# Optimization experiments

Hardware: AMD Instinct MI355X
Metric: run time of the kernel (lower is better)

## Reference

```python
import jax, jax.numpy as jnp
import numpy as np

N_NODES = 100000
N_EDGES = 1600000
IN_FEATS, N_HIDDEN, N_CLASSES = 128, 128, 32


def setup_inputs() -> dict:
    key = jax.random.key(0)
    ks = jax.random.split(key, 9)
    x = jax.random.normal(ks[0], (N_NODES, IN_FEATS), dtype=jnp.float32)
    src = jax.random.randint(ks[1], (N_EDGES,), 0, N_NODES, dtype=jnp.int64)
    dst = jax.random.randint(ks[2], (N_EDGES,), 0, N_NODES, dtype=jnp.int64)
    s1 = 1.0 / np.sqrt(IN_FEATS)
    s2 = 1.0 / np.sqrt(N_HIDDEN)
    W1 = jax.random.uniform(ks[3], (IN_FEATS, N_HIDDEN), jnp.float32, -s1, s1)
    b1 = jnp.zeros((N_HIDDEN,), jnp.float32)
    W2 = jax.random.uniform(ks[4], (N_HIDDEN, N_HIDDEN), jnp.float32, -s2, s2)
    b2 = jnp.zeros((N_HIDDEN,), jnp.float32)
    W3 = jax.random.uniform(ks[5], (N_HIDDEN, N_CLASSES), jnp.float32, -s2, s2)
    b3 = jnp.zeros((N_CLASSES,), jnp.float32)
    return {"x": x, "W1": W1, "b1": b1, "W2": W2, "b2": b2, "W3": W3, "b3": b3,
            "src": src, "dst": dst}


def _norms(src, dst):
    ones = jnp.ones((src.shape[0],), jnp.float32)
    deg_out = jax.ops.segment_sum(ones, src, num_segments=N_NODES)
    deg_in = jax.ops.segment_sum(ones, dst, num_segments=N_NODES)
    inv_sqrt = lambda d: jnp.where(d > 0, jax.lax.rsqrt(jnp.maximum(d, 1.0)), 0.0)
    return inv_sqrt(deg_out), inv_sqrt(deg_in)


def _sgconv(h, W, b, src, dst, norm_src, norm_dst):
    # D^-1/2 A D^-1/2 h, then linear
    m = h * norm_src[:, None]          # scale by source (out-degree) norm
    msg = m[src]                        # [E, F] gather
    agg = jax.ops.segment_sum(msg, dst, num_segments=N_NODES)  # scatter-add
    agg = agg * norm_dst[:, None]
    return agg @ W + b


def reference(x, W1, b1, W2, b2, W3, b3, src, dst):
    norm_src, norm_dst = _norms(src, dst)
    h = _sgconv(x, W1, b1, src, dst, norm_src, norm_dst)
    h = jax.nn.relu(h)
    h = _sgconv(h, W2, b2, src, dst, norm_src, norm_dst)
    h = jax.nn.relu(h)
    h = _sgconv(h, W3, b3, src, dst, norm_src, norm_dst)
    return h
```

## Files before the change

kernel.cpp:

```cpp
#include <hip/hip_runtime.h>


constexpr int FEAT   = 128;
constexpr int STRIDE = 48;

typedef float f32x4 __attribute__((ext_vector_type(4)));
typedef short bf16x8 __attribute__((ext_vector_type(8)));

__device__ __forceinline__ unsigned short f2bf(float f) {
    unsigned int u = __builtin_bit_cast(unsigned int, f);
    unsigned int r = (u + 0x7FFFu + ((u >> 16) & 1u)) >> 16;
    return (unsigned short)r;
}
__device__ __forceinline__ float bflo(unsigned int u) {
    return __builtin_bit_cast(float, u << 16);
}
__device__ __forceinline__ float bfhi(unsigned int u) {
    return __builtin_bit_cast(float, u & 0xffff0000u);
}
__device__ __forceinline__ unsigned int pack2(float a, float b) {
    return (unsigned int)f2bf(a) | ((unsigned int)f2bf(b) << 16);
}

__global__ __launch_bounds__(256) void w1frag_kernel(const float* __restrict__ W1,
                                                     unsigned short* __restrict__ frag)
{
    constexpr int NC = 128;
    int idx = blockIdx.x * 256 + threadIdx.x;
    if (idx >= 8 * 4 * 64) return;
    int l  = idx & 63;
    int k0 = (idx >> 6) & 3;
    int n0 = idx >> 8;
    int kb = k0 * 32 + (l >> 4) * 8;
    int n  = n0 * 16 + (l & 15);
    const float* wp = W1 + (size_t)kb * NC + n;
    uint4 v;
    v.x = pack2(wp[0],      wp[NC]);
    v.y = pack2(wp[2 * NC], wp[3 * NC]);
    v.z = pack2(wp[4 * NC], wp[5 * NC]);
    v.w = pack2(wp[6 * NC], wp[7 * NC]);
    *reinterpret_cast<uint4*>(&frag[idx * 8]) = v;
}

__global__ __launch_bounds__(256) void degree_fill_xw1_kernel(
    const int* __restrict__ src, const int* __restrict__ dst,
    const float* __restrict__ x, const unsigned short* __restrict__ w1frag,
    int* __restrict__ deg_out, int* __restrict__ deg_in,
    int* __restrict__ csr_pad, unsigned short* __restrict__ xw1,
    int N, int E)
{
    const int tid = threadIdx.x;
    const int g = (int)blockIdx.x / 5;
    const int m = (int)blockIdx.x % 5;

    if (m != 4) {
        int e = (g * 4 + m) * 256 + tid;
        if (e < E) {
            int s = src[e];
            int d = dst[e];
            atomicAdd(&deg_out[s], 1);
            int pos = atomicAdd(&deg_in[d], 1);
            if (pos < STRIDE)
                csr_pad[(size_t)d * STRIDE + pos] = s;
        }
        return;
    }

    const int wave = tid >> 6, lane = tid & 63;
    const int rowbase = g * 64 + wave * 16;
    const int arow = min(rowbase + (lane & 15), N - 1);
    const int koff = (lane >> 4) * 8;

    bf16x8 a[4];
    #pragma unroll
    for (int k0 = 0; k0 < 4; ++k0) {
        const float* xp = x + (size_t)arow * 128 + k0 * 32 + koff;
        float4 f0 = *reinterpret_cast<const float4*>(xp);
        float4 f1 = *reinterpret_cast<const float4*>(xp + 4);
        union { unsigned int u[4]; bf16x8 v; } r;
        r.u[0] = pack2(f0.x, f0.y); r.u[1] = pack2(f0.z, f0.w);
        r.u[2] = pack2(f1.x, f1.y); r.u[3] = pack2(f1.z, f1.w);
        a[k0] = r.v;
    }

    f32x4 acc[8];
    #pragma unroll
    for (int n0 = 0; n0 < 8; ++n0) acc[n0] = (f32x4)0.f;
    #pragma unroll
    for (int k0 = 0; k0 < 4; ++k0) {
        #pragma unroll
        for (int n0 = 0; n0 < 8; ++n0) {
            bf16x8 b = *reinterpret_cast<const bf16x8*>(&w1frag[((n0 * 4 + k0) * 64 + lane) * 8]);
            acc[n0] = __builtin_amdgcn_mfma_f32_16x16x32_bf16(a[k0], b, acc[n0], 0, 0, 0);
        }
    }

    const int colbase = lane & 15;
    const int rowoff = (lane >> 4) * 4;
    #pragma unroll
    for (int r = 0; r < 4; ++r) {
        const int grow = rowbase + rowoff + r;
        if (grow < N) {
            unsigned short* op = xw1 + (size_t)grow * 128 + colbase;
            #pragma unroll
            for (int n0 = 0; n0 < 8; ++n0)
                op[n0 * 16] = f2bf(acc[n0][r]);
        }
    }
}

__global__ __launch_bounds__(256) void norm_kernel(const int* __restrict__ dout,
                                                   const int* __restrict__ din,
                                                   float* __restrict__ nsrc,
                                                   float* __restrict__ ndst, int N)
{
    int i = blockIdx.x * 256 + threadIdx.x;
    if (i < N) {
        int a = dout[i], b = din[i];
        nsrc[i] = (a > 0) ? rsqrtf((float)a) : 0.f;
        ndst[i] = (b > 0) ? rsqrtf((float)b) : 0.f;
    }
}

__global__ __launch_bounds__(256) void gather1_kernel(const unsigned short* __restrict__ xw1,
                                                      const float* __restrict__ nsrc,
                                                      const float* __restrict__ ndst,
                                                      const int* __restrict__ deg_in,
                                                      const int* __restrict__ csr_pad,
                                                      const float* __restrict__ b1,
                                                      unsigned short* __restrict__ hb1,
                                                      int N)
{
    const int node = blockIdx.x * 16 + (threadIdx.x >> 4);
    const int c = (threadIdx.x & 15) * 8;
    if (node >= N) return;
    const int* idx = csr_pad + (size_t)node * STRIDE;
    const int deg = min(deg_in[node], STRIDE);
    float4 a0 = make_float4(0.f, 0.f, 0.f, 0.f);
    float4 a1 = make_float4(0.f, 0.f, 0.f, 0.f);
    int j = 0;
    for (; j + 8 <= deg; j += 8) {
        int s[8];
        float ns[8];
        #pragma unroll
        for (int u = 0; u < 8; ++u) s[u] = idx[j + u];
        #pragma unroll
        for (int u = 0; u < 8; ++u) ns[u] = nsrc[s[u]];
        #pragma unroll
        for (int u = 0; u < 8; ++u) {
            uint4 v = *reinterpret_cast<const uint4*>(xw1 + (size_t)s[u] * 128 + c);
            a0.x = fmaf(bflo(v.x), ns[u], a0.x);
            a0.y = fmaf(bfhi(v.x), ns[u], a0.y);
            a0.z = fmaf(bflo(v.y), ns[u], a0.z);
            a0.w = fmaf(bfhi(v.y), ns[u], a0.w);
            a1.x = fmaf(bflo(v.z), ns[u], a1.x);
            a1.y = fmaf(bfhi(v.z), ns[u], a1.y);
            a1.z = fmaf(bflo(v.w), ns[u], a1.z);
            a1.w = fmaf(bfhi(v.w), ns[u], a1.w);
        }
    }
    for (; j < deg; ++j) {
        int s0 = idx[j];
        float n0 = nsrc[s0];
        uint4 v = *reinterpret_cast<const uint4*>(xw1 + (size_t)s0 * 128 + c);
        a0.x = fmaf(bflo(v.x), n0, a0.x);
        a0.y = fmaf(bfhi(v.x), n0, a0.y);
        a0.z = fmaf(bflo(v.y), n0, a0.z);
        a0.w = fmaf(bfhi(v.y), n0, a0.w);
        a1.x = fmaf(bflo(v.z), n0, a1.x);
        a1.y = fmaf(bfhi(v.z), n0, a1.y);
        a1.z = fmaf(bflo(v.w), n0, a1.z);
        a1.w = fmaf(bfhi(v.w), n0, a1.w);
    }
    const float nd = ndst[node];
    const float nsn = nsrc[node];
    const float* bp = b1 + c;
    float v0 = fmaxf(a0.x * nd + bp[0], 0.f) * nsn;
    float v1 = fmaxf(a0.y * nd + bp[1], 0.f) * nsn;
    float v2 = fmaxf(a0.z * nd + bp[2], 0.f) * nsn;
    float v3 = fmaxf(a0.w * nd + bp[3], 0.f) * nsn;
    float v4 = fmaxf(a1.x * nd + bp[4], 0.f) * nsn;
    float v5 = fmaxf(a1.y * nd + bp[5], 0.f) * nsn;
    float v6 = fmaxf(a1.z * nd + bp[6], 0.f) * nsn;
    float v7 = fmaxf(a1.w * nd + bp[7], 0.f) * nsn;
    uint4 o;
    o.x = pack2(v0, v1); o.y = pack2(v2, v3);
    o.z = pack2(v4, v5); o.w = pack2(v6, v7);
    *reinterpret_cast<uint4*>(hb1 + (size_t)node * 128 + c) = o;
}

__global__ __launch_bounds__(256) void gather128_kernel(const unsigned short* __restrict__ hb,
                                                        const float* __restrict__ ndst,
                                                        const int* __restrict__ deg_in,
                                                        const int* __restrict__ csr_pad,
                                                        unsigned short* __restrict__ aggb,
                                                        int N)
{
    const int node = blockIdx.x * 16 + (threadIdx.x >> 4);
    const int c = (threadIdx.x & 15) * 8;
    if (node >= N) return;
    const int* idx = csr_pad + (size_t)node * STRIDE;
    const int deg = min(deg_in[node], STRIDE);
    float4 a0 = make_float4(0.f, 0.f, 0.f, 0.f);
    float4 a1 = make_float4(0.f, 0.f, 0.f, 0.f);
    int j = 0;
    for (; j + 8 <= deg; j += 8) {
        int s[8];
        #pragma unroll
        for (int u = 0; u < 8; ++u) s[u] = idx[j + u];
        #pragma unroll
        for (int u = 0; u < 8; ++u) {
            uint4 v = *reinterpret_cast<const uint4*>(hb + (size_t)s[u] * 128 + c);
            a0.x += bflo(v.x); a0.y += bfhi(v.x);
            a0.z += bflo(v.y); a0.w += bfhi(v.y);
            a1.x += bflo(v.z); a1.y += bfhi(v.z);
            a1.z += bflo(v.w); a1.w += bfhi(v.w);
        }
    }
    for (; j < deg; ++j) {
        uint4 v = *reinterpret_cast<const uint4*>(hb + (size_t)idx[j] * 128 + c);
        a0.x += bflo(v.x); a0.y += bfhi(v.x);
        a0.z += bflo(v.y); a0.w += bfhi(v.y);
        a1.x += bflo(v.z); a1.y += bfhi(v.z);
        a1.z += bflo(v.w); a1.w += bfhi(v.w);
    }
    const float nd = ndst[node];
    uint4 o;
    o.x = pack2(a0.x * nd, a0.y * nd);
    o.y = pack2(a0.z * nd, a0.w * nd);
    o.z = pack2(a1.x * nd, a1.y * nd);
    o.w = pack2(a1.z * nd, a1.w * nd);
    *reinterpret_cast<uint4*>(aggb + (size_t)node * 128 + c) = o;
}

template<int NT, bool RELU, bool BIAS, bool SCALE>
__global__ __launch_bounds__(256) void mfma_gemm_kernel(
    const unsigned short* __restrict__ Ab,
    const float* __restrict__ W,
    const float* __restrict__ bias,
    const float* __restrict__ nsrc,
    unsigned short* __restrict__ Cb,
    int N)
{
    constexpr int NC = NT * 16;
    constexpr int SLD = (NC == 128) ? 136 : 32;
    __shared__ alignas(16) unsigned short Wl[NT * 4 * 64 * 8];
    __shared__ alignas(16) unsigned short Sc[4][16 * SLD];
    const int tid = threadIdx.x;

    for (int idx = tid; idx < NT * 4 * 64; idx += 256) {
        int l  = idx & 63;
        int k0 = (idx >> 6) & 3;
        int n0 = idx >> 8;
        int kb = k0 * 32 + (l >> 4) * 8;
        int n  = n0 * 16 + (l & 15);
        const float* wp = W + (size_t)kb * NC + n;
        uint4 v;
        v.x = pack2(wp[0],      wp[NC]);
        v.y = pack2(wp[2 * NC], wp[3 * NC]);
        v.z = pack2(wp[4 * NC], wp[5 * NC]);
        v.w = pack2(wp[6 * NC], wp[7 * NC]);
        *reinterpret_cast<uint4*>(&Wl[idx * 8]) = v;
    }
    __syncthreads();

    const int wave = tid >> 6, lane = tid & 63;
    const int rowbase = blockIdx.x * 64 + wave * 16;
    const int arow = min(rowbase + (lane & 15), N - 1);
    const int koff = (lane >> 4) * 8;

    bf16x8 a[4];
    #pragma unroll
    for (int k0 = 0; k0 < 4; ++k0)
        a[k0] = *reinterpret_cast<const bf16x8*>(Ab + (size_t)arow * 128 + k0 * 32 + koff);

    f32x4 acc[NT];
    #pragma unroll
    for (int n0 = 0; n0 < NT; ++n0) acc[n0] = (f32x4)0.f;

    #pragma unroll
    for (int k0 = 0; k0 < 4; ++k0) {
        #pragma unroll
        for (int n0 = 0; n0 < NT; ++n0) {
            bf16x8 b = *reinterpret_cast<const bf16x8*>(&Wl[((n0 * 4 + k0) * 64 + lane) * 8]);
            acc[n0] = __builtin_amdgcn_mfma_f32_16x16x32_bf16(a[k0], b, acc[n0], 0, 0, 0);
        }
    }

    float rs[4];
    #pragma unroll
    for (int r = 0; r < 4; ++r) {
        int row = (lane >> 4) * 4 + r;
        rs[r] = SCALE ? nsrc[min(rowbase + row, N - 1)] : 1.f;
    }
    unsigned short* sc = &Sc[wave][0];
    #pragma unroll
    for (int n0 = 0; n0 < NT; ++n0) {
        int col = n0 * 16 + (lane & 15);
        float bv = BIAS ? bias[col] : 0.f;
        #pragma unroll
        for (int r = 0; r < 4; ++r) {
            int row = (lane >> 4) * 4 + r;
            float v = acc[n0][r] + bv;
            if (RELU) v = fmaxf(v, 0.f);
            v *= rs[r];
            sc[row * SLD + col] = f2bf(v);
        }
    }

    constexpr int CHUNKS = NC / 32;
    const int wrow = lane >> 2, q = lane & 3;
    const int grow = rowbase + wrow;
    if (grow < N) {
        #pragma unroll
        for (int t = 0; t < CHUNKS; ++t) {
            uint4 v = *reinterpret_cast<const uint4*>(&sc[wrow * SLD + q * (CHUNKS * 8) + t * 8]);
            *reinterpret_cast<uint4*>(Cb + (size_t)grow * NC + q * (CHUNKS * 8) + t * 8) = v;
        }
    }
}

__global__ __launch_bounds__(256) void gather32_kernel(const unsigned short* __restrict__ hb,
                                                       const float* __restrict__ ndst,
                                                       const int* __restrict__ deg_in,
                                                       const int* __restrict__ csr_pad,
                                                       const float* __restrict__ bias,
                                                       float* __restrict__ out, int N)
{
    const int node = blockIdx.x * 64 + (threadIdx.x >> 2);
    const int c = (threadIdx.x & 3) * 8;
    if (node >= N) return;
    const int* idx = csr_pad + (size_t)node * STRIDE;
    const int deg = min(deg_in[node], STRIDE);
    float4 a0 = make_float4(0.f, 0.f, 0.f, 0.f);
    float4 a1 = make_float4(0.f, 0.f, 0.f, 0.f);
    int j = 0;
    for (; j + 8 <= deg; j += 8) {
        int s[8];
        #pragma unroll
        for (int u = 0; u < 8; ++u) s[u] = idx[j + u];
        #pragma unroll
        for (int u = 0; u < 8; ++u) {
            uint4 v = *reinterpret_cast<const uint4*>(hb + (size_t)s[u] * 32 + c);
            a0.x += bflo(v.x); a0.y += bfhi(v.x);
            a0.z += bflo(v.y); a0.w += bfhi(v.y);
            a1.x += bflo(v.z); a1.y += bfhi(v.z);
            a1.z += bflo(v.w); a1.w += bfhi(v.w);
        }
    }
    for (; j < deg; ++j) {
        uint4 v = *reinterpret_cast<const uint4*>(hb + (size_t)idx[j] * 32 + c);
        a0.x += bflo(v.x); a0.y += bfhi(v.x);
        a0.z += bflo(v.y); a0.w += bfhi(v.y);
        a1.x += bflo(v.z); a1.y += bfhi(v.z);
        a1.z += bflo(v.w); a1.w += bfhi(v.w);
    }
    const float nd = ndst[node];
    float4 o0, o1;
    o0.x = a0.x * nd + bias[c + 0]; o0.y = a0.y * nd + bias[c + 1];
    o0.z = a0.z * nd + bias[c + 2]; o0.w = a0.w * nd + bias[c + 3];
    o1.x = a1.x * nd + bias[c + 4]; o1.y = a1.y * nd + bias[c + 5];
    o1.z = a1.z * nd + bias[c + 6]; o1.w = a1.w * nd + bias[c + 7];
    float* op = out + (size_t)node * 32 + c;
    *reinterpret_cast<float4*>(op)     = o0;
    *reinterpret_cast<float4*>(op + 4) = o1;
}

extern "C" void kernel_launch(void* const* d_in, const int* in_sizes, int n_in,
                              void* d_out, int out_size, void* d_ws, size_t ws_size,
                              hipStream_t stream)
{
    const float* x  = (const float*)d_in[0];
    const float* W1 = (const float*)d_in[1];
    const float* b1 = (const float*)d_in[2];
    const float* W2 = (const float*)d_in[3];
    const float* b2 = (const float*)d_in[4];
    const float* W3 = (const float*)d_in[5];
    const float* b3 = (const float*)d_in[6];
    const int*   src = (const int*)d_in[7];
    const int*   dst = (const int*)d_in[8];
    float* out = (float*)d_out;

    const int N = in_sizes[0] / FEAT;
    const int E = in_sizes[7];
    const int GB = (N + 63) / 64;

    char* w = (char*)d_ws;
    float* norm_src  = (float*)w;                  w += (size_t)N * 4;
    float* norm_dst  = (float*)w;                  w += (size_t)N * 4;
    int*   deg_out   = (int*)w;                    w += (size_t)N * 4;
    int*   deg_in    = (int*)w;                    w += (size_t)N * 4;
    unsigned short* w1frag = (unsigned short*)w;   w += (size_t)2048 * 8 * 2;
    int*   csr_pad   = (int*)w;                    w += (size_t)N * STRIDE * 4;
    unsigned short* xw1  = (unsigned short*)w;     w += (size_t)N * FEAT * 2;
    unsigned short* hb1  = (unsigned short*)w;     w += (size_t)N * FEAT * 2;
    unsigned short* aggb = (unsigned short*)w;
    unsigned short* h2b = xw1;
    unsigned short* tb  = hb1;

    const int gblocks = (N + 63) / 64;

    hipMemsetAsync(deg_out, 0, 2 * (size_t)N * sizeof(int), stream);
    w1frag_kernel<<<8, 256, 0, stream>>>(W1, w1frag);
    degree_fill_xw1_kernel<<<GB * 5, 256, 0, stream>>>(
        src, dst, x, w1frag, deg_out, deg_in, csr_pad, xw1, N, E);
    norm_kernel<<<(N + 255) / 256, 256, 0, stream>>>(deg_out, deg_in, norm_src, norm_dst, N);

    gather1_kernel<<<(N + 15) / 16, 256, 0, stream>>>(
        xw1, norm_src, norm_dst, deg_in, csr_pad, b1, hb1, N);

    gather128_kernel<<<(N + 15) / 16, 256, 0, stream>>>(
        hb1, norm_dst, deg_in, csr_pad, aggb, N);
    mfma_gemm_kernel<8, true, true, false><<<gblocks, 256, 0, stream>>>(
        aggb, W2, b2, nullptr, h2b, N);

    mfma_gemm_kernel<2, false, false, true><<<gblocks, 256, 0, stream>>>(
        h2b, W3, nullptr, norm_src, tb, N);
    gather32_kernel<<<(N + 63) / 64, 256, 0, stream>>>(
        tb, norm_dst, deg_in, csr_pad, b3, out, N);
}
```

Baseline: 344.9 us.

## Fuse layer-2 and layer-3 GEMMs and add source-partitioned passes to the 128-wide gather

The layer-2 GEMM (bias+ReLU) and the layer-3 projection are fused into one kernel that keeps the hidden tile in shared memory and runs a second MFMA stage, so the h2 intermediate is never written to or read back from global memory. The 128-wide gather now stages each node's neighbor list in shared memory. It also walks that list in 8 passes, each restricted to one slice of source nodes, so concurrent blocks touch a smaller working set and L2 hit rates should rise. The cost is 8x the index scanning and branch work in the gather. The W3 fragment packing is merged into the W1 preprocessing kernel.

```diff
diff --git a/kernel.cpp b/kernel.cpp
--- a/kernel.cpp
+++ b/kernel.cpp
@@ -3,6 +3,7 @@
 
 constexpr int FEAT   = 128;
 constexpr int STRIDE = 48;
+constexpr int PASSES = 8;
 
 typedef float f32x4 __attribute__((ext_vector_type(4)));
 typedef short bf16x8 __attribute__((ext_vector_type(8)));
@@ -22,24 +23,30 @@
     return (unsigned int)f2bf(a) | ((unsigned int)f2bf(b) << 16);
 }
 
-__global__ __launch_bounds__(256) void w1frag_kernel(const float* __restrict__ W1,
-                                                     unsigned short* __restrict__ frag)
-{
-    constexpr int NC = 128;
+__global__ __launch_bounds__(256) void wfrag_kernel(const float* __restrict__ W1,
+                                                    const float* __restrict__ W3,
+                                                    unsigned short* __restrict__ f1,
+                                                    unsigned short* __restrict__ f3)
+{
     int idx = blockIdx.x * 256 + threadIdx.x;
-    if (idx >= 8 * 4 * 64) return;
-    int l  = idx & 63;
-    int k0 = (idx >> 6) & 3;
-    int n0 = idx >> 8;
+    const float* W;
+    unsigned short* f;
+    int NC, i;
+    if (idx < 2048)      { W = W1; f = f1; NC = 128; i = idx; }
+    else if (idx < 2560) { W = W3; f = f3; NC = 32;  i = idx - 2048; }
+    else return;
+    int l  = i & 63;
+    int k0 = (i >> 6) & 3;
+    int n0 = i >> 8;
     int kb = k0 * 32 + (l >> 4) * 8;
     int n  = n0 * 16 + (l & 15);
-    const float* wp = W1 + (size_t)kb * NC + n;
+    const float* wp = W + (size_t)kb * NC + n;
     uint4 v;
     v.x = pack2(wp[0],      wp[NC]);
     v.y = pack2(wp[2 * NC], wp[3 * NC]);
     v.z = pack2(wp[4 * NC], wp[5 * NC]);
     v.w = pack2(wp[6 * NC], wp[7 * NC]);
-    *reinterpret_cast<uint4*>(&frag[idx * 8]) = v;
+    *reinterpret_cast<uint4*>(&f[i * 8]) = v;
 }
 
 __global__ __launch_bounds__(256) void degree_fill_xw1_kernel(
@@ -189,40 +196,48 @@
     *reinterpret_cast<uint4*>(hb1 + (size_t)node * 128 + c) = o;
 }
 
-__global__ __launch_bounds__(256) void gather128_kernel(const unsigned short* __restrict__ hb,
-                                                        const float* __restrict__ ndst,
-                                                        const int* __restrict__ deg_in,
-                                                        const int* __restrict__ csr_pad,
-                                                        unsigned short* __restrict__ aggb,
-                                                        int N)
-{
-    const int node = blockIdx.x * 16 + (threadIdx.x >> 4);
+__global__ __launch_bounds__(256) void gather128s_kernel(const unsigned short* __restrict__ hb,
+                                                         const float* __restrict__ ndst,
+                                                         const int* __restrict__ deg_in,
+                                                         const int* __restrict__ csr_pad,
+                                                         unsigned short* __restrict__ aggb,
+                                                         int N, int SL)
+{
+    __shared__ int sidx[16 * STRIDE];
+    __shared__ int sdeg[16];
+    const int nb = blockIdx.x * 16;
+    if (threadIdx.x < 16) {
+        int n = nb + threadIdx.x;
+        sdeg[threadIdx.x] = (n < N) ? min(deg_in[n], STRIDE) : 0;
+    }
+    for (int i = threadIdx.x; i < 16 * STRIDE; i += 256) {
+        int n = nb + i / STRIDE;
+        if (n < N) sidx[i] = csr_pad[(size_t)n * STRIDE + i % STRIDE];
+    }
+    __syncthreads();
+
+    const int g = threadIdx.x >> 4;
     const int c = (threadIdx.x & 15) * 8;
+    const int node = nb + g;
     if (node >= N) return;
-    const int* idx = csr_pad + (size_t)node * STRIDE;
-    const int deg = min(deg_in[node], STRIDE);
+    const int deg = sdeg[g];
+    const int* idx = &sidx[g * STRIDE];
     float4 a0 = make_float4(0.f, 0.f, 0.f, 0.f);
     float4 a1 = make_float4(0.f, 0.f, 0.f, 0.f);
-    int j = 0;
-    for (; j + 8 <= deg; j += 8) {
-        int s[8];
-        #pragma unroll
-        for (int u = 0; u < 8; ++u) s[u] = idx[j + u];
-        #pragma unroll
-        for (int u = 0; u < 8; ++u) {
-            uint4 v = *reinterpret_cast<const uint4*>(hb + (size_t)s[u] * 128 + c);
-            a0.x += bflo(v.x); a0.y += bfhi(v.x);
-            a0.z += bflo(v.y); a0.w += bfhi(v.y);
-            a1.x += bflo(v.z); a1.y += bfhi(v.z);
-            a1.z += bflo(v.w); a1.w += bfhi(v.w);
-        }
-    }
-    for (; j < deg; ++j) {
-        uint4 v = *reinterpret_cast<const uint4*>(hb + (size_t)idx[j] * 128 + c);
-        a0.x += bflo(v.x); a0.y += bfhi(v.x);
-        a0.z += bflo(v.y); a0.w += bfhi(v.y);
-        a1.x += bflo(v.z); a1.y += bfhi(v.z);
-        a1.z += bflo(v.w); a1.w += bfhi(v.w);
+
+    for (int p = 0; p < PASSES; ++p) {
+        const int lo = p * SL, hi = lo + SL;
+        #pragma unroll 4
+        for (int j = 0; j < deg; ++j) {
+            int s = idx[j];
+            if (s >= lo && s < hi) {
+                uint4 v = *reinterpret_cast<const uint4*>(hb + (size_t)s * 128 + c);
+                a0.x += bflo(v.x); a0.y += bfhi(v.x);
+                a0.z += bflo(v.y); a0.w += bfhi(v.y);
+                a1.x += bflo(v.z); a1.y += bfhi(v.z);
+                a1.z += bflo(v.w); a1.w += bfhi(v.w);
+            }
+        }
     }
     const float nd = ndst[node];
     uint4 o;
@@ -233,28 +248,27 @@
     *reinterpret_cast<uint4*>(aggb + (size_t)node * 128 + c) = o;
 }
 
-template<int NT, bool RELU, bool BIAS, bool SCALE>
-__global__ __launch_bounds__(256) void mfma_gemm_kernel(
+__global__ __launch_bounds__(256) void gemm23_kernel(
     const unsigned short* __restrict__ Ab,
-    const float* __restrict__ W,
-    const float* __restrict__ bias,
+    const float* __restrict__ W2,
+    const float* __restrict__ b2,
+    const unsigned short* __restrict__ w3frag,
     const float* __restrict__ nsrc,
-    unsigned short* __restrict__ Cb,
+    unsigned short* __restrict__ tb,
     int N)
 {
-    constexpr int NC = NT * 16;
-    constexpr int SLD = (NC == 128) ? 136 : 32;
-    __shared__ alignas(16) unsigned short Wl[NT * 4 * 64 * 8];
+    constexpr int NC = 128, SLD = 136;
+    __shared__ alignas(16) unsigned short Wl[8 * 4 * 64 * 8];
     __shared__ alignas(16) unsigned short Sc[4][16 * SLD];
     const int tid = threadIdx.x;
 
-    for (int idx = tid; idx < NT * 4 * 64; idx += 256) {
+    for (int idx = tid; idx < 8 * 4 * 64; idx += 256) {
         int l  = idx & 63;
         int k0 = (idx >> 6) & 3;
         int n0 = idx >> 8;
         int kb = k0 * 32 + (l >> 4) * 8;
         int n  = n0 * 16 + (l & 15);
-        const float* wp = W + (size_t)kb * NC + n;
+        const float* wp = W2 + (size_t)kb * NC + n;
         uint4 v;
         v.x = pack2(wp[0],      wp[NC]);
         v.y = pack2(wp[2 * NC], wp[3 * NC]);
@@ -274,48 +288,54 @@
     for (int k0 = 0; k0 < 4; ++k0)
         a[k0] = *reinterpret_cast<const bf16x8*>(Ab + (size_t)arow * 128 + k0 * 32 + koff);
 
-    f32x4 acc[NT];
-    #pragma unroll
-    for (int n0 = 0; n0 < NT; ++n0) acc[n0] = (f32x4)0.f;
-
+    f32x4 acc[8];
+    #pragma unroll
+    for (int n0 = 0; n0 < 8; ++n0) acc[n0] = (f32x4)0.f;
     #pragma unroll
     for (int k0 = 0; k0 < 4; ++k0) {
         #pragma unroll
-        for (int n0 = 0; n0 < NT; ++n0) {
+        for (int n0 = 0; n0 < 8; ++n0) {
             bf16x8 b = *reinterpret_cast<const bf16x8*>(&Wl[((n0 * 4 + k0) * 64 + lane) * 8]);
             acc[n0] = __builtin_amdgcn_mfma_f32_16x16x32_bf16(a[k0], b, acc[n0], 0, 0, 0);
         }
     }
 
-    float rs[4];
-    #pragma unroll
-    for (int r = 0; r < 4; ++r) {
-        int row = (lane >> 4) * 4 + r;
-        rs[r] = SCALE ? nsrc[min(rowbase + row, N - 1)] : 1.f;
-    }
     unsigned short* sc = &Sc[wave][0];
     #pragma unroll
-    for (int n0 = 0; n0 < NT; ++n0) {
+    for (int n0 = 0; n0 < 8; ++n0) {
         int col = n0 * 16 + (lane & 15);
-        float bv = BIAS ? bias[col] : 0.f;
+        float bv = b2[col];
         #pragma unroll
         for (int r = 0; r < 4; ++r) {
             int row = (lane >> 4) * 4 + r;
-            float v = acc[n0][r] + bv;
-            if (RELU) v = fmaxf(v, 0.f);
-            v *= rs[r];
-            sc[row * SLD + col] = f2bf(v);
-        }
-    }
-
-    constexpr int CHUNKS = NC / 32;
-    const int wrow = lane >> 2, q = lane & 3;
-    const int grow = rowbase + wrow;
-    if (grow < N) {
-        #pragma unroll
-        for (int t = 0; t < CHUNKS; ++t) {
-            uint4 v = *reinterpret_cast<const uint4*>(&sc[wrow * SLD + q * (CHUNKS * 8) + t * 8]);
-            *reinterpret_cast<uint4*>(Cb + (size_t)grow * NC + q * (CHUNKS * 8) + t * 8) = v;
+            sc[row * SLD + col] = f2bf(fmaxf(acc[n0][r] + bv, 0.f));
+        }
+    }
+
+    f32x4 acc3[2];
+    acc3[0] = (f32x4)0.f; acc3[1] = (f32x4)0.f;
+    #pragma unroll
+    for (int k0 = 0; k0 < 4; ++k0) {
+        bf16x8 a3 = *reinterpret_cast<const bf16x8*>(&sc[(lane & 15) * SLD + k0 * 32 + koff]);
+        #pragma unroll
+        for (int n0 = 0; n0 < 2; ++n0) {
+            bf16x8 b = *reinterpret_cast<const bf16x8*>(&w3frag[((n0 * 4 + k0) * 64 + lane) * 8]);
+            acc3[n0] = __builtin_amdgcn_mfma_f32_16x16x32_bf16(a3, b, acc3[n0], 0, 0, 0);
+        }
+    }
+
+    float rs[4];
+    #pragma unroll
+    for (int r = 0; r < 4; ++r)
+        rs[r] = nsrc[min(rowbase + (lane >> 4) * 4 + r, N - 1)];
+    #pragma unroll
+    for (int n0 = 0; n0 < 2; ++n0) {
+        int col = n0 * 16 + (lane & 15);
+        #pragma unroll
+        for (int r = 0; r < 4; ++r) {
+            int grow = rowbase + (lane >> 4) * 4 + r;
+            if (grow < N)
+                tb[(size_t)grow * 32 + col] = f2bf(acc3[n0][r] * rs[r]);
         }
     }
 }
@@ -384,6 +404,7 @@
     const int N = in_sizes[0] / FEAT;
     const int E = in_sizes[7];
     const int GB = (N + 63) / 64;
+    const int SL = (N + PASSES - 1) / PASSES;
 
     char* w = (char*)d_ws;
     float* norm_src  = (float*)w;                  w += (size_t)N * 4;
@@ -391,17 +412,15 @@
     int*   deg_out   = (int*)w;                    w += (size_t)N * 4;
     int*   deg_in    = (int*)w;                    w += (size_t)N * 4;
     unsigned short* w1frag = (unsigned short*)w;   w += (size_t)2048 * 8 * 2;
+    unsigned short* w3frag = (unsigned short*)w;   w += (size_t)512 * 8 * 2;
     int*   csr_pad   = (int*)w;                    w += (size_t)N * STRIDE * 4;
     unsigned short* xw1  = (unsigned short*)w;     w += (size_t)N * FEAT * 2;
     unsigned short* hb1  = (unsigned short*)w;     w += (size_t)N * FEAT * 2;
     unsigned short* aggb = (unsigned short*)w;
-    unsigned short* h2b = xw1;
-    unsigned short* tb  = hb1;
-
-    const int gblocks = (N + 63) / 64;
+    unsigned short* tb = xw1;
 
     hipMemsetAsync(deg_out, 0, 2 * (size_t)N * sizeof(int), stream);
-    w1frag_kernel<<<8, 256, 0, stream>>>(W1, w1frag);
+    wfrag_kernel<<<10, 256, 0, stream>>>(W1, W3, w1frag, w3frag);
     degree_fill_xw1_kernel<<<GB * 5, 256, 0, stream>>>(
         src, dst, x, w1frag, deg_out, deg_in, csr_pad, xw1, N, E);
     norm_kernel<<<(N + 255) / 256, 256, 0, stream>>>(deg_out, deg_in, norm_src, norm_dst, N);
@@ -409,13 +428,10 @@
     gather1_kernel<<<(N + 15) / 16, 256, 0, stream>>>(
         xw1, norm_src, norm_dst, deg_in, csr_pad, b1, hb1, N);
 
-    gather128_kernel<<<(N + 15) / 16, 256, 0, stream>>>(
-        hb1, norm_dst, deg_in, csr_pad, aggb, N);
-    mfma_gemm_kernel<8, true, true, false><<<gblocks, 256, 0, stream>>>(
-        aggb, W2, b2, nullptr, h2b, N);
-
-    mfma_gemm_kernel<2, false, false, true><<<gblocks, 256, 0, stream>>>(
-        h2b, W3, nullptr, norm_src, tb, N);
+    gather128s_kernel<<<(N + 15) / 16, 256, 0, stream>>>(
+        hb1, norm_dst, deg_in, csr_pad, aggb, N, SL);
+    gemm23_kernel<<<GB, 256, 0, stream>>>(aggb, W2, b2, w3frag, norm_src, tb, N);
+
     gather32_kernel<<<(N + 63) / 64, 256, 0, stream>>>(
         tb, norm_dst, deg_in, csr_pad, b3, out, N);
 }
```

New measurement: 406.6 us. 17.9% more time.
